# Performance work log

Measured on AMD Instinct MI355X. Metric: run time of the kernel, lower is better.

Reference implementation:

```python
import jax, jax.numpy as jnp
import numpy as np

NUM_EXPERTS = 8
PHM_DIM = 4


def setup_inputs() -> dict:
    key = jax.random.key(0)
    k1, k2, k3, k4 = jax.random.split(key, 4)
    bsz, seq, D, O, E, p = 4, 2048, 2048, 2048, NUM_EXPERTS, PHM_DIM
    hidden_states = jax.random.normal(k1, (bsz, seq, D), dtype=jnp.float32)
    gate_w = jax.random.normal(k2, (D, E), dtype=jnp.float32) * 0.02
    phm_rule = jax.random.normal(k3, (E, p, p, p), dtype=jnp.float32) * 0.1
    W = jax.random.normal(k4, (E, p, D // p, O // p), dtype=jnp.float32) * 0.02
    b = jnp.zeros((E, O), dtype=jnp.float32)
    return {"hidden_states": hidden_states, "gate_w": gate_w,
            "phm_rule": phm_rule, "W": W, "b": b}


def reference(hidden_states, gate_w, phm_rule, W, b):
    bsz, seq, dim = hidden_states.shape
    E = gate_w.shape[1]
    x = hidden_states.reshape(-1, dim)                      # [T, D]
    logits = x @ gate_w                                     # [T, E]
    prob = jax.nn.softmax(logits, axis=-1)                  # [T, E]
    gate = jnp.argmax(prob, axis=-1)                        # [T]
    # load-balancing loss
    num_tokens = jnp.sum(jax.nn.one_hot(gate, E, dtype=jnp.int32), axis=0)  # [E]
    f = num_tokens.astype(prob.dtype)
    f = f / jnp.sum(f)
    P = jnp.mean(prob, axis=0)
    balance_loss = E * jnp.sum(P * f)
    # PHM weight per expert: H_e = sum_p kron(phm_rule[e,p], W[e,p]) -> [E, D, O]
    Wfull = jnp.einsum('epab,epij->eaibj', phm_rule, W).reshape(E, dim, -1)
    # dense evaluation of every expert on every token, then top-1 select
    all_out = jnp.einsum('td,edo->teo', x, Wfull) + b[None, :, :]  # [T, E, O]
    tok_prob = jnp.take_along_axis(prob, gate[:, None], axis=1)    # [T, 1]
    out = jnp.take_along_axis(all_out, gate[:, None, None], axis=1)[:, 0, :] * tok_prob
    out = out.reshape(bsz, seq, -1)
    return out, balance_loss, num_tokens
```

## Files before the change

kernel.cpp:

```cpp
#include <hip/hip_runtime.h>
#include <cstdint>
#include <cstddef>

typedef _Float16 f16;
typedef f16 f16x2 __attribute__((ext_vector_type(2)));
typedef f16 f16x4 __attribute__((ext_vector_type(4)));
typedef f16 f16x8 __attribute__((ext_vector_type(8)));
typedef float f32x4 __attribute__((ext_vector_type(4)));

#define NEXP 8
#define BM 128
#define BN 128
#define BK 32
#define NSTAGE 3

__device__ __forceinline__ void async_cp16(void* lds, const void* gsrc) {
  __builtin_amdgcn_global_load_lds(
      (const __attribute__((address_space(1))) void*)gsrc,
      (__attribute__((address_space(3))) void*)lds, 16, 0, 0);
}

__global__ __launch_bounds__(256) void k_gwT(const float* __restrict__ gw,
                                             float* __restrict__ gwT, int D) {
  int i = blockIdx.x * 256 + threadIdx.x;
  int e = i / D, d = i - e * D;
  gwT[i] = gw[d * NEXP + e];
}

__global__ __launch_bounds__(256) void k_gate(
    const float* __restrict__ x, const float* __restrict__ gwT,
    f16* __restrict__ xb, int* __restrict__ gate, float* __restrict__ scale,
    int* __restrict__ cnt, float* __restrict__ probsum, int D)
{
  __shared__ float ps[NEXP];
  __shared__ int pc[NEXP];
  int tid = threadIdx.x, lane = tid & 63, w = tid >> 6;
  if (tid < NEXP) { ps[tid] = 0.f; pc[tid] = 0; }
  __syncthreads();

  int t = blockIdx.x * 4 + w;
  const float* xr = x + (size_t)t * D;
  f16* xbr = xb + (size_t)t * D;

  float acc[NEXP] = {};
  for (int d0 = lane * 4; d0 < D; d0 += 256) {
    float4 v = *(const float4*)(xr + d0);
    f16x4 h; h[0] = (f16)v.x; h[1] = (f16)v.y; h[2] = (f16)v.z; h[3] = (f16)v.w;
    *(f16x4*)(xbr + d0) = h;
#pragma unroll
    for (int e = 0; e < NEXP; e++) {
      float4 g = *(const float4*)(gwT + (size_t)e * D + d0);
      acc[e] += v.x * g.x + v.y * g.y + v.z * g.z + v.w * g.w;
    }
  }
#pragma unroll
  for (int e = 0; e < NEXP; e++) {
    float v = acc[e];
    for (int o = 32; o > 0; o >>= 1) v += __shfl_xor(v, o);
    acc[e] = v;
  }
  if (lane == 0) {
    float m = acc[0]; int g = 0;
#pragma unroll
    for (int e = 1; e < NEXP; e++) if (acc[e] > m) { m = acc[e]; g = e; }
    float pr[NEXP]; float ssum = 0.f;
#pragma unroll
    for (int e = 0; e < NEXP; e++) { pr[e] = __expf(acc[e] - m); ssum += pr[e]; }
    float inv = 1.0f / ssum;
#pragma unroll
    for (int e = 0; e < NEXP; e++) atomicAdd(&ps[e], pr[e] * inv);
    atomicAdd(&pc[g], 1);
    gate[t] = g;
    scale[t] = pr[g] * inv;
  }
  __syncthreads();
  if (tid < NEXP) {
    atomicAdd(&probsum[tid], ps[tid]);
    atomicAdd(&cnt[tid], pc[tid]);
  }
}

__global__ __launch_bounds__(256) void k_wfull(
    const float* __restrict__ Wp, const float* __restrict__ rule,
    f16* __restrict__ wt, int Dp, int Op, int D, int O)
{
  int bid = blockIdx.x;
  int it = Dp >> 5, jt = Op >> 5;
  int itile = bid % it; bid /= it;
  int jtile = bid % jt; bid /= jt;
  int e = bid;
  int i0 = itile * 32, j0 = jtile * 32;

  __shared__ float Wt[4][32][33];
  int tid = threadIdx.x;
  for (int idx = tid; idx < 4096; idx += 256) {
    int p = idx >> 10, rem = idx & 1023, ii = rem >> 5, jj = rem & 31;
    Wt[p][ii][jj] = Wp[(size_t)((e * 4 + p) * Dp + i0 + ii) * Op + j0 + jj];
  }
  __syncthreads();

  int ii = (tid & 15) * 2, jjb = tid >> 4;
#pragma unroll
  for (int b = 0; b < 4; b++) {
    float s[4][4];
#pragma unroll
    for (int p = 0; p < 4; p++)
#pragma unroll
      for (int a = 0; a < 4; a++)
        s[p][a] = rule[((e * 4 + p) * 4 + a) * 4 + b];
#pragma unroll
    for (int a = 0; a < 4; a++) {
#pragma unroll
      for (int jp = 0; jp < 2; jp++) {
        int jj = jjb + jp * 16;
        float v0 = 0.f, v1 = 0.f;
#pragma unroll
        for (int p = 0; p < 4; p++) {
          v0 += s[p][a] * Wt[p][ii][jj];
          v1 += s[p][a] * Wt[p][ii + 1][jj];
        }
        size_t n = (size_t)b * Op + j0 + jj;
        size_t dd = (size_t)a * Dp + i0 + ii;
        f16x2 hv; hv[0] = (f16)v0; hv[1] = (f16)v1;
        *(f16x2*)(wt + ((size_t)e * O + n) * D + dd) = hv;
      }
    }
  }
}

__global__ __launch_bounds__(128) void k_plan(
    const int* __restrict__ cnt, const float* __restrict__ probsum,
    int* __restrict__ offs, int* __restrict__ ndesc,
    int2* __restrict__ desc, float* __restrict__ otail, int T)
{
  __shared__ int soffs[NEXP + 1];
  __shared__ int snd;
  __shared__ float sloss;
  __shared__ int2 sdesc[96];
  int tid = threadIdx.x;
  if (tid == 0) {
    int off = 0, nd = 0; float loss = 0.f;
    for (int e = 0; e < NEXP; e++) {
      soffs[e] = off;
      int c = cnt[e];
      loss += probsum[e] * (float)c;
      for (int m0 = 0; m0 < c; m0 += BM) { sdesc[nd] = make_int2(e, m0); nd++; }
      off += c;
    }
    soffs[NEXP] = off;
    snd = nd;
    sloss = loss;
  }
  __syncthreads();
  if (tid <= NEXP) offs[tid] = soffs[tid];
  if (tid == 9) *ndesc = snd;
  if (tid == 10) {
    float invT = 1.0f / (float)T;
    otail[0] = (float)NEXP * sloss * invT * invT;
  }
  if (tid >= 16 && tid < 16 + NEXP) otail[1 + tid - 16] = (float)cnt[tid - 16];
  for (int i = tid; i < snd; i += 128) desc[i] = sdesc[i];
}

__global__ __launch_bounds__(256) void k_scatter(
    const int* __restrict__ gate, const int* __restrict__ offs,
    int* __restrict__ cursor, int* __restrict__ perm)
{
  int t = blockIdx.x * 256 + threadIdx.x;
  int g = gate[t];
  int lane = threadIdx.x & 63;
  int pos = 0;
#pragma unroll
  for (int e = 0; e < NEXP; e++) {
    unsigned long long mask = __ballot(g == e);
    if (mask == 0ull) continue;
    int leader = __ffsll((unsigned long long)mask) - 1;
    int base = 0;
    if (lane == leader) base = atomicAdd(&cursor[e], (int)__popcll(mask));
    base = __shfl(base, leader);
    if (g == e) {
      int below = (int)__popcll(mask & ((1ull << lane) - 1ull));
      pos = offs[e] + base + below;
    }
  }
  perm[pos] = t;
}

__global__ __launch_bounds__(256) void k_gemm(
    const f16* __restrict__ xb, const f16* __restrict__ wt,
    const float* __restrict__ bias, const int* __restrict__ perm,
    const int* __restrict__ cnt, const int* __restrict__ offs,
    const int* __restrict__ ndesc, const int2* __restrict__ desc,
    const float* __restrict__ scale, float* __restrict__ out, int D, int O)
{
  if ((int)blockIdx.y >= *ndesc) return;
  int2 dsc = desc[blockIdx.y];
  int e = dsc.x, m0 = dsc.y;
  int ce = cnt[e];
  int seg = offs[e];
  int n0 = blockIdx.x * BN;

  __shared__ f16 Al[NSTAGE][BM * BK];
  __shared__ f16 Bl[NSTAGE][BN * BK];
  __shared__ int tokS[BM];
  __shared__ float scS[BM];

  int tid = threadIdx.x;
  if (tid < BM) {
    int idx = m0 + tid; if (idx > ce - 1) idx = ce - 1;
    int tok = perm[seg + idx];
    tokS[tid] = tok;
    scS[tid] = scale[tok];
  }
  __syncthreads();

  int r = tid >> 2;
  int c = tid & 3;
  int gc = c ^ ((r >> 1) & 3);
  const f16* a1 = xb + (size_t)tokS[r] * D + gc * 8;
  const f16* a2 = xb + (size_t)tokS[r + 64] * D + gc * 8;
  const f16* b1 = wt + ((size_t)e * O + n0 + r) * D + gc * 8;
  const f16* b2 = wt + ((size_t)e * O + n0 + r + 64) * D + gc * 8;

  int lane = tid & 63;
  int w = tid >> 6;
  int wm = (w & 1) * 64, wn = (w >> 1) * 64;
  int lr = lane & 15, q = lane >> 4;
  int qs = q ^ ((lr >> 1) & 3);

  f32x4 acc[4][4] = {};
  int nk = D / BK;

#define STAGE(kk, p)                                             \
  do {                                                           \
    async_cp16(&Al[(p)][tid * 8], a1 + (kk) * BK);               \
    async_cp16(&Al[(p)][2048 + tid * 8], a2 + (kk) * BK);        \
    async_cp16(&Bl[(p)][tid * 8], b1 + (kk) * BK);               \
    async_cp16(&Bl[(p)][2048 + tid * 8], b2 + (kk) * BK);        \
  } while (0)

  STAGE(0, 0);
  STAGE(1, 1);
  STAGE(2, 2);

  int p = 0;
  for (int kk = 0; kk < nk; ++kk) {
    int rem = nk - 1 - kk;
    if (rem >= 2)
      asm volatile("s_waitcnt vmcnt(8)\n\ts_barrier" ::: "memory");
    else if (rem == 1)
      asm volatile("s_waitcnt vmcnt(4)\n\ts_barrier" ::: "memory");
    else
      asm volatile("s_waitcnt vmcnt(0)\n\ts_barrier" ::: "memory");

    f16x8 af[4], bf[4];
#pragma unroll
    for (int mi = 0; mi < 4; mi++)
      af[mi] = *(const f16x8*)&Al[p][(wm + mi * 16 + lr) * BK + qs * 8];
#pragma unroll
    for (int ni = 0; ni < 4; ni++)
      bf[ni] = *(const f16x8*)&Bl[p][(wn + ni * 16 + lr) * BK + qs * 8];

    asm volatile("s_waitcnt lgkmcnt(0)\n\ts_barrier" ::: "memory");
    if (kk + NSTAGE < nk) STAGE(kk + NSTAGE, p);

#pragma unroll
    for (int mi = 0; mi < 4; mi++)
#pragma unroll
      for (int ni = 0; ni < 4; ni++)
        acc[mi][ni] = __builtin_amdgcn_mfma_f32_16x16x32_f16(
            af[mi], bf[ni], acc[mi][ni], 0, 0, 0);

    p++; if (p == NSTAGE) p = 0;
  }
#undef STAGE

  float bv[4];
#pragma unroll
  for (int ni = 0; ni < 4; ni++)
    bv[ni] = bias[(size_t)e * O + n0 + wn + ni * 16 + lr];
#pragma unroll
  for (int mi = 0; mi < 4; mi++) {
#pragma unroll
    for (int rg = 0; rg < 4; rg++) {
      int rl = wm + mi * 16 + q * 4 + rg;
      if (m0 + rl < ce) {
        float s = scS[rl];
        float* orow = out + (size_t)tokS[rl] * O + n0 + wn;
#pragma unroll
        for (int ni = 0; ni < 4; ni++)
          orow[ni * 16 + lr] = (acc[mi][ni][rg] + bv[ni]) * s;
      }
    }
  }
}

extern "C" void kernel_launch(void* const* d_in, const int* in_sizes, int n_in,
                              void* d_out, int out_size, void* d_ws, size_t ws_size,
                              hipStream_t stream)
{
  const float* x    = (const float*)d_in[0];
  const float* gw   = (const float*)d_in[1];
  const float* rule = (const float*)d_in[2];
  const float* W    = (const float*)d_in[3];
  const float* bias = (const float*)d_in[4];
  float* out = (float*)d_out;

  int D = in_sizes[1] / NEXP;
  int O = in_sizes[4] / NEXP;
  int T = in_sizes[0] / D;
  int Dp = D / 4, Op = O / 4;

  uint8_t* ws = (uint8_t*)d_ws;
  size_t off = 0;
  f16* xb = (f16*)(ws + off);  off += (size_t)T * D * 2;
  f16* wt = (f16*)(ws + off);  off += (size_t)NEXP * O * D * 2;
  int*   gate  = (int*)(ws + off);   off += (size_t)T * 4;
  float* scale = (float*)(ws + off); off += (size_t)T * 4;
  int*   perm  = (int*)(ws + off);   off += (size_t)T * 4;
  off = (off + 255) & ~(size_t)255;
  uint8_t* C = ws + off;
  int*   cnt     = (int*)(C + 0);
  float* probsum = (float*)(C + 32);
  int*   cursor  = (int*)(C + 64);
  int*   ndesc   = (int*)(C + 96);
  int*   offs    = (int*)(C + 128);
  int2*  desc    = (int2*)(C + 192);
  float* gwT     = (float*)(C + 4096);

  hipMemsetAsync(C, 0, 128, stream);

  k_gwT<<<(NEXP * D) / 256, 256, 0, stream>>>(gw, gwT, D);
  k_gate<<<T / 4, 256, 0, stream>>>(x, gwT, xb, gate, scale, cnt, probsum, D);
  k_wfull<<<NEXP * (Op / 32) * (Dp / 32), 256, 0, stream>>>(W, rule, wt, Dp, Op, D, O);
  k_plan<<<1, 128, 0, stream>>>(cnt, probsum, offs, ndesc, desc, out + (size_t)T * O, T);
  k_scatter<<<T / 256, 256, 0, stream>>>(gate, offs, cursor, perm);

  int maxdesc = T / BM + NEXP;
  k_gemm<<<dim3(O / BN, maxdesc), 256, 0, stream>>>(
      xb, wt, bias, perm, cnt, offs, ndesc, desc, scale, out, D, O);
}
```

Before: 339.6 us.

## Enlarge expert GEMM tiles to 256x256 with interleaved LDS reads and MFMA

The grouped expert GEMM moves from 128x128x32 tiles with 256 threads and a 3-stage ring to 256x256x64 tiles with 512 threads and double buffering. Each wave now computes a 128x64 sub-tile, splitting its LDS fragment reads into chunks interleaved with MFMA groups wrapped in s_setprio. A new XOR swizzle covers the wider K slice. The aim is more operand reuse per byte loaded and better overlap of LDS and global traffic with matrix math. The cost is far fewer blocks (tail imbalance across CUs, more padded rows per expert segment), heavy LDS use per block and high register pressure.

Result: slower. 354.3 us (+4.3%).

```diff
diff --git a/kernel.cpp b/kernel.cpp
--- a/kernel.cpp
+++ b/kernel.cpp
@@ -9,10 +9,9 @@
 typedef float f32x4 __attribute__((ext_vector_type(4)));
 
 #define NEXP 8
-#define BM 128
-#define BN 128
-#define BK 32
-#define NSTAGE 3
+#define BM 256
+#define BN 256
+#define BK 64
 
 __device__ __forceinline__ void async_cp16(void* lds, const void* gsrc) {
   __builtin_amdgcn_global_load_lds(
@@ -186,7 +185,7 @@
   perm[pos] = t;
 }
 
-__global__ __launch_bounds__(256) void k_gemm(
+__global__ __launch_bounds__(512) void k_gemm(
     const f16* __restrict__ xb, const f16* __restrict__ wt,
     const float* __restrict__ bias, const int* __restrict__ perm,
     const int* __restrict__ cnt, const int* __restrict__ offs,
@@ -200,8 +199,8 @@
   int seg = offs[e];
   int n0 = blockIdx.x * BN;
 
-  __shared__ f16 Al[NSTAGE][BM * BK];
-  __shared__ f16 Bl[NSTAGE][BN * BK];
+  __shared__ f16 As[2][BM * BK];
+  __shared__ f16 Bs[2][BN * BK];
   __shared__ int tokS[BM];
   __shared__ float scS[BM];
 
@@ -214,79 +213,128 @@
   }
   __syncthreads();
 
-  int r = tid >> 2;
-  int c = tid & 3;
-  int gc = c ^ ((r >> 1) & 3);
-  const f16* a1 = xb + (size_t)tokS[r] * D + gc * 8;
-  const f16* a2 = xb + (size_t)tokS[r + 64] * D + gc * 8;
-  const f16* b1 = wt + ((size_t)e * O + n0 + r) * D + gc * 8;
-  const f16* b2 = wt + ((size_t)e * O + n0 + r + 64) * D + gc * 8;
+  int sr = tid >> 3, sc = tid & 7;
+  uint32_t offA[4], offB[4];
+#pragma unroll
+  for (int rr = 0; rr < 4; rr++) {
+    int row = sr + rr * 64;
+    int gc = sc ^ (row & 7);
+    offA[rr] = ((uint32_t)tokS[row] * (uint32_t)D + (uint32_t)(gc * 8)) * 2u;
+    offB[rr] = ((uint32_t)(e * O + n0 + row) * (uint32_t)D + (uint32_t)(gc * 8)) * 2u;
+  }
+
+#define STAGE(kk, pb)                                                         \
+  do {                                                                        \
+    _Pragma("unroll")                                                         \
+    for (int rr = 0; rr < 4; rr++)                                            \
+      async_cp16(&As[pb][rr * 4096 + tid * 8],                                \
+                 (const char*)xb + offA[rr] + (kk) * (BK * 2));               \
+    _Pragma("unroll")                                                         \
+    for (int rr = 0; rr < 4; rr++)                                            \
+      async_cp16(&Bs[pb][rr * 4096 + tid * 8],                                \
+                 (const char*)wt + offB[rr] + (kk) * (BK * 2));               \
+  } while (0)
 
   int lane = tid & 63;
-  int w = tid >> 6;
-  int wm = (w & 1) * 64, wn = (w >> 1) * 64;
+  int wid = tid >> 6;
+  int wr = wid >> 2, wc = wid & 3;
   int lr = lane & 15, q = lane >> 4;
-  int qs = q ^ ((lr >> 1) & 3);
-
-  f32x4 acc[4][4] = {};
-  int nk = D / BK;
-
-#define STAGE(kk, p)                                             \
-  do {                                                           \
-    async_cp16(&Al[(p)][tid * 8], a1 + (kk) * BK);               \
-    async_cp16(&Al[(p)][2048 + tid * 8], a2 + (kk) * BK);        \
-    async_cp16(&Bl[(p)][tid * 8], b1 + (kk) * BK);               \
-    async_cp16(&Bl[(p)][2048 + tid * 8], b2 + (kk) * BK);        \
-  } while (0)
+  int aoff = (wr * 128 + lr) * BK;
+  int boff = (wc * 64 + lr) * BK;
+  int s0 = ((q ^ (lr & 7)) * 8);
+  int s1 = s0 ^ 32;
+
+  f32x4 acc[8][4] = {};
+  int nkt = D / BK;
 
   STAGE(0, 0);
   STAGE(1, 1);
-  STAGE(2, 2);
-
-  int p = 0;
-  for (int kk = 0; kk < nk; ++kk) {
-    int rem = nk - 1 - kk;
-    if (rem >= 2)
-      asm volatile("s_waitcnt vmcnt(8)\n\ts_barrier" ::: "memory");
-    else if (rem == 1)
-      asm volatile("s_waitcnt vmcnt(4)\n\ts_barrier" ::: "memory");
-    else
-      asm volatile("s_waitcnt vmcnt(0)\n\ts_barrier" ::: "memory");
-
-    f16x8 af[4], bf[4];
-#pragma unroll
-    for (int mi = 0; mi < 4; mi++)
-      af[mi] = *(const f16x8*)&Al[p][(wm + mi * 16 + lr) * BK + qs * 8];
-#pragma unroll
-    for (int ni = 0; ni < 4; ni++)
-      bf[ni] = *(const f16x8*)&Bl[p][(wn + ni * 16 + lr) * BK + qs * 8];
-
-    asm volatile("s_waitcnt lgkmcnt(0)\n\ts_barrier" ::: "memory");
-    if (kk + NSTAGE < nk) STAGE(kk + NSTAGE, p);
-
+  asm volatile("s_waitcnt vmcnt(8)\n\ts_barrier" ::: "memory");
+
+#pragma unroll 2
+  for (int kt = 0; kt < nkt; ++kt) {
+    int p = kt & 1;
+    const f16* Ab = As[p];
+    const f16* Bb = Bs[p];
+    f16x8 a0[4], a1[4], a2[4], a3[4], b0[4], b1[4];
+
+#pragma unroll
+    for (int i = 0; i < 4; i++) {
+      a0[i] = *(const f16x8*)&Ab[aoff + (i * 16) * BK + s0];
+      b0[i] = *(const f16x8*)&Bb[boff + (i * 16) * BK + s0];
+    }
+#pragma unroll
+    for (int i = 0; i < 4; i++)
+      a1[i] = *(const f16x8*)&Ab[aoff + ((i + 4) * 16) * BK + s0];
+
+    __builtin_amdgcn_s_setprio(1);
 #pragma unroll
     for (int mi = 0; mi < 4; mi++)
 #pragma unroll
       for (int ni = 0; ni < 4; ni++)
         acc[mi][ni] = __builtin_amdgcn_mfma_f32_16x16x32_f16(
-            af[mi], bf[ni], acc[mi][ni], 0, 0, 0);
-
-    p++; if (p == NSTAGE) p = 0;
+            a0[mi], b0[ni], acc[mi][ni], 0, 0, 0);
+    __builtin_amdgcn_s_setprio(0);
+
+#pragma unroll
+    for (int i = 0; i < 4; i++) {
+      a2[i] = *(const f16x8*)&Ab[aoff + (i * 16) * BK + s1];
+      b1[i] = *(const f16x8*)&Bb[boff + (i * 16) * BK + s1];
+    }
+
+    __builtin_amdgcn_s_setprio(1);
+#pragma unroll
+    for (int mi = 0; mi < 4; mi++)
+#pragma unroll
+      for (int ni = 0; ni < 4; ni++)
+        acc[mi + 4][ni] = __builtin_amdgcn_mfma_f32_16x16x32_f16(
+            a1[mi], b0[ni], acc[mi + 4][ni], 0, 0, 0);
+    __builtin_amdgcn_s_setprio(0);
+
+#pragma unroll
+    for (int i = 0; i < 4; i++)
+      a3[i] = *(const f16x8*)&Ab[aoff + ((i + 4) * 16) * BK + s1];
+
+    __builtin_amdgcn_s_setprio(1);
+#pragma unroll
+    for (int mi = 0; mi < 4; mi++)
+#pragma unroll
+      for (int ni = 0; ni < 4; ni++)
+        acc[mi][ni] = __builtin_amdgcn_mfma_f32_16x16x32_f16(
+            a2[mi], b1[ni], acc[mi][ni], 0, 0, 0);
+    __builtin_amdgcn_s_setprio(0);
+
+    asm volatile("s_waitcnt lgkmcnt(0)\n\ts_barrier" ::: "memory");
+    if (kt + 2 < nkt) STAGE(kt + 2, p);
+
+    __builtin_amdgcn_s_setprio(1);
+#pragma unroll
+    for (int mi = 0; mi < 4; mi++)
+#pragma unroll
+      for (int ni = 0; ni < 4; ni++)
+        acc[mi + 4][ni] = __builtin_amdgcn_mfma_f32_16x16x32_f16(
+            a3[mi], b1[ni], acc[mi + 4][ni], 0, 0, 0);
+    __builtin_amdgcn_s_setprio(0);
+
+    if (kt + 2 < nkt)
+      asm volatile("s_waitcnt vmcnt(8)\n\ts_barrier" ::: "memory");
+    else if (kt + 1 < nkt)
+      asm volatile("s_waitcnt vmcnt(0)\n\ts_barrier" ::: "memory");
   }
 #undef STAGE
 
   float bv[4];
 #pragma unroll
   for (int ni = 0; ni < 4; ni++)
-    bv[ni] = bias[(size_t)e * O + n0 + wn + ni * 16 + lr];
-#pragma unroll
-  for (int mi = 0; mi < 4; mi++) {
+    bv[ni] = bias[(size_t)e * O + n0 + wc * 64 + ni * 16 + lr];
+#pragma unroll
+  for (int mi = 0; mi < 8; mi++) {
 #pragma unroll
     for (int rg = 0; rg < 4; rg++) {
-      int rl = wm + mi * 16 + q * 4 + rg;
+      int rl = wr * 128 + mi * 16 + q * 4 + rg;
       if (m0 + rl < ce) {
         float s = scS[rl];
-        float* orow = out + (size_t)tokS[rl] * O + n0 + wn;
+        float* orow = out + (size_t)tokS[rl] * O + n0 + wc * 64;
 #pragma unroll
         for (int ni = 0; ni < 4; ni++)
           orow[ni * 16 + lr] = (acc[mi][ni][rg] + bv[ni]) * s;
@@ -337,6 +385,6 @@
   k_scatter<<<T / 256, 256, 0, stream>>>(gate, offs, cursor, perm);
 
   int maxdesc = T / BM + NEXP;
-  k_gemm<<<dim3(O / BN, maxdesc), 256, 0, stream>>>(
+  k_gemm<<<dim3(O / BN, maxdesc), 512, 0, stream>>>(
       xb, wt, bias, perm, cnt, offs, ndesc, desc, scale, out, D, O);
 }
```
